# Optimization experiments

Measured on AMD Instinct MI355X. Metric: run time of the kernel, lower is better.

Reference implementation:

```python
import jax, jax.numpy as jnp
import numpy as np

N_NODES = 20000
OUT_DEG = 16
E = N_NODES * OUT_DEG          # 320000 directed edges
F = 20                          # edge_features
H3 = 3 * F


def _lin(key, fan_in, fan_out):
    kw, kb = jax.random.split(key)
    bound = 1.0 / np.sqrt(fan_in)
    W = jax.random.uniform(kw, (fan_in, fan_out), jnp.float32, -bound, bound)
    b = jax.random.uniform(kb, (fan_out,), jnp.float32, -bound, bound)
    return W, b


def setup_inputs() -> dict:
    key = jax.random.key(0)
    rng = np.random.default_rng(0)
    # graph: every node has exactly OUT_DEG out-edges, no self-loops
    src = np.repeat(np.arange(N_NODES, dtype=np.int64), OUT_DEG)
    dst = (src + 1 + rng.integers(0, N_NODES - 1, size=E)) % N_NODES
    edge_index = jnp.asarray(np.stack([src, dst]), dtype=jnp.int32)
    # edge adjacency per _build_edge_adj: edge i=(u->v) pairs with each out-edge j of v.
    # Edges are grouped by src, so out-edges of node v are [v*OUT_DEG, v*OUT_DEG+OUT_DEG).
    # No self-loops => i != j always, so exactly E*OUT_DEG pairs.
    adj_src = jnp.asarray(np.repeat(np.arange(E, dtype=np.int64), OUT_DEG).astype(np.int32))
    adj_nbr = jnp.asarray((dst[:, None] * OUT_DEG + np.arange(OUT_DEG)).reshape(-1).astype(np.int32))

    ks = jax.random.split(key, 8)
    edge_attr = jax.random.normal(ks[0], (E, F), jnp.float32)
    msg_W1, msg_b1 = _lin(ks[1], 2 * F, 32)
    msg_W2, msg_b2 = _lin(ks[2], 32, F)
    # torch GRUCell params: weight_ih/hh are [3H, H]
    bound = 1.0 / np.sqrt(F)
    g = jax.random.split(ks[3], 4)
    gru_Wih = jax.random.uniform(g[0], (H3, F), jnp.float32, -bound, bound)
    gru_Whh = jax.random.uniform(g[1], (H3, F), jnp.float32, -bound, bound)
    gru_bih = jax.random.uniform(g[2], (H3,), jnp.float32, -bound, bound)
    gru_bhh = jax.random.uniform(g[3], (H3,), jnp.float32, -bound, bound)
    ro_W1, ro_b1 = _lin(ks[4], F, 64)
    ro_W2, ro_b2 = _lin(ks[5], 64, 32)
    ro_W3, ro_b3 = _lin(ks[6], 32, 1)
    return {
        'edge_attr': edge_attr,
        'msg_W1': msg_W1, 'msg_b1': msg_b1, 'msg_W2': msg_W2, 'msg_b2': msg_b2,
        'gru_Wih': gru_Wih, 'gru_Whh': gru_Whh, 'gru_bih': gru_bih, 'gru_bhh': gru_bhh,
        'ro_W1': ro_W1, 'ro_b1': ro_b1, 'ro_W2': ro_W2, 'ro_b2': ro_b2,
        'ro_W3': ro_W3, 'ro_b3': ro_b3,
        'edge_index': edge_index, 'adj_src': adj_src, 'adj_nbr': adj_nbr,
    }


def reference(edge_attr, msg_W1, msg_b1, msg_W2, msg_b2,
              gru_Wih, gru_Whh, gru_bih, gru_bhh,
              ro_W1, ro_b1, ro_W2, ro_b2, ro_W3, ro_b3,
              edge_index, adj_src, adj_nbr):
    num_e = edge_attr.shape[0]

    def step(h, _):
        h_i = h[adj_src]                       # [P, F] gather
        h_j = h[adj_nbr]                       # [P, F] gather
        m = jnp.concatenate([h_i, h_j], axis=-1)  # [P, 2F]
        m = jax.nn.selu(m @ msg_W1 + msg_b1) @ msg_W2 + msg_b2  # [P, F]
        agg = jax.ops.segment_sum(m, adj_src, num_segments=num_e)  # scatter_add
        # torch.nn.GRUCell(agg, h)
        gi = agg @ gru_Wih.T + gru_bih
        gh = h @ gru_Whh.T + gru_bhh
        i_r, i_z, i_n = jnp.split(gi, 3, axis=-1)
        h_r, h_z, h_n = jnp.split(gh, 3, axis=-1)
        r = jax.nn.sigmoid(i_r + h_r)
        z = jax.nn.sigmoid(i_z + h_z)
        n = jnp.tanh(i_n + r * h_n)
        return (1.0 - z) * n + z * h, None

    h_t, _ = jax.lax.scan(step, edge_attr, None, length=4)
    h_base = h_t[:num_e]  # num_edges == E here
    x = jax.nn.selu(h_base @ ro_W1 + ro_b1)
    x = jax.nn.selu(x @ ro_W2 + ro_b2)
    w = jax.nn.softplus(x @ ro_W3 + ro_b3).squeeze(-1) + 0.1
    return jnp.clip(w, 0.1, 10.0)
```

## Files before the change

### kernel.cpp

```cpp
#include <hip/hip_runtime.h>
#include <hip/hip_fp16.h>

#define E_EDGES 320000
#define NF 20

typedef float v4 __attribute__((ext_vector_type(4)));
typedef float v2f __attribute__((ext_vector_type(2)));

#if defined(__has_builtin)
# if __has_builtin(__builtin_elementwise_fma)
#  define EWFMA(a,b,c) __builtin_elementwise_fma((a),(b),(c))
# endif
#endif
#ifndef EWFMA
# define EWFMA(a,b,c) ((a)*(b)+(c))
#endif
#if defined(__has_builtin)
# if __has_builtin(__builtin_elementwise_max)
#  define EWMAX(a,b) __builtin_elementwise_max((a),(b))
#  define EWMIN(a,b) __builtin_elementwise_min((a),(b))
# endif
#endif

__device__ __forceinline__ v4 bc4(float s) { return (v4){s, s, s, s}; }
__device__ __forceinline__ v4 v4z() { return (v4){0.f, 0.f, 0.f, 0.f}; }

__device__ __forceinline__ float selu_f(float x) {
    const float scale = 1.0507009873554805f;
    const float alpha = 1.6732632423543772f;
    float p = fmaxf(x, 0.f);
    float m = fminf(x, 0.f);
    float e = __expf(m);
    return fmaf(scale, p, scale * alpha * (e - 1.f));
}
__device__ __forceinline__ float sigmoid_f(float x) {
    return 1.f / (1.f + __expf(-x));
}
__device__ __forceinline__ v4 selu4(v4 x) {
    const float scale = 1.0507009873554805f;
    const float ka = 1.0507009873554805f * 1.6732632423543772f;
#ifdef EWMAX
    v4 p = EWMAX(x, v4z());
    v4 m = EWMIN(x, v4z());
#else
    v4 p = {fmaxf(x.x,0.f), fmaxf(x.y,0.f), fmaxf(x.z,0.f), fmaxf(x.w,0.f)};
    v4 m = {fminf(x.x,0.f), fminf(x.y,0.f), fminf(x.z,0.f), fminf(x.w,0.f)};
#endif
    v4 e = {__expf(m.x), __expf(m.y), __expf(m.z), __expf(m.w)};
    return EWFMA(bc4(scale), p, EWFMA(bc4(ka), e, bc4(-ka)));
}

__device__ __forceinline__ float hsum4(v4 x) {
    v2f lo = __builtin_shufflevector(x, x, 0, 1);
    v2f hi = __builtin_shufflevector(x, x, 2, 3);
    v2f h = lo + hi;
    return h.x + h.y;
}

__device__ __forceinline__ float dot20v(v4 a0, v4 a1, v4 a2, v4 a3, v4 a4,
                                        const v4* __restrict__ w) {
    v4 w0 = w[0], w1 = w[1], w2 = w[2], w3 = w[3], w4 = w[4];
    v4 x = a0 * w0;
    x = EWFMA(a1, w1, x); x = EWFMA(a2, w2, x);
    x = EWFMA(a3, w3, x); x = EWFMA(a4, w4, x);
    return hsum4(x);
}
__device__ __forceinline__ void dot20_dualv(const v4* __restrict__ w,
    v4 a0, v4 a1, v4 a2, v4 a3, v4 a4,
    v4 b0, v4 b1, v4 b2, v4 b3, v4 b4,
    float& r0, float& r1)
{
    v4 w0 = w[0], w1 = w[1], w2 = w[2], w3 = w[3], w4 = w[4];
    v4 xa = a0 * w0;
    xa = EWFMA(a1, w1, xa); xa = EWFMA(a2, w2, xa);
    xa = EWFMA(a3, w3, xa); xa = EWFMA(a4, w4, xa);
    v4 xb = b0 * w0;
    xb = EWFMA(b1, w1, xb); xb = EWFMA(b2, w2, xb);
    xb = EWFMA(b3, w3, xb); xb = EWFMA(b4, w4, xb);
    r0 = hsum4(xa);
    r1 = hsum4(xb);
}
__device__ __forceinline__ void h8_to_v4x2(uint4 r, v4& lo, v4& hi) {
    float2 fa = __half22float2(__builtin_bit_cast(__half2, r.x));
    float2 fb = __half22float2(__builtin_bit_cast(__half2, r.y));
    float2 fc = __half22float2(__builtin_bit_cast(__half2, r.z));
    float2 fd = __half22float2(__builtin_bit_cast(__half2, r.w));
    lo = (v4){fa.x, fa.y, fb.x, fb.y};
    hi = (v4){fc.x, fc.y, fd.x, fd.y};
}
__device__ __forceinline__ uint4 f8_to_h8(v4 lo, v4 hi) {
    uint4 r;
    r.x = __builtin_bit_cast(unsigned, __floats2half2_rn(lo.x, lo.y));
    r.y = __builtin_bit_cast(unsigned, __floats2half2_rn(lo.z, lo.w));
    r.z = __builtin_bit_cast(unsigned, __floats2half2_rn(hi.x, hi.y));
    r.w = __builtin_bit_cast(unsigned, __floats2half2_rn(hi.z, hi.w));
    return r;
}

#define FOR20(X) \
  X(0, v0.x) X(1, v0.y) X(2, v0.z) X(3, v0.w) \
  X(4, v1.x) X(5, v1.y) X(6, v1.z) X(7, v1.w) \
  X(8, v2.x) X(9, v2.y) X(10, v2.z) X(11, v2.w) \
  X(12, v3.x) X(13, v3.y) X(14, v3.z) X(15, v3.w) \
  X(16, v4v.x) X(17, v4v.y) X(18, v4v.z) X(19, v4v.w)

#define FOR20_2(X) \
  X(0, va0.x, vb0.x) X(1, va0.y, vb0.y) X(2, va0.z, vb0.z) X(3, va0.w, vb0.w) \
  X(4, va1.x, vb1.x) X(5, va1.y, vb1.y) X(6, va1.z, vb1.z) X(7, va1.w, vb1.w) \
  X(8, va2.x, vb2.x) X(9, va2.y, vb2.y) X(10, va2.z, vb2.z) X(11, va2.w, vb2.w) \
  X(12, va3.x, vb3.x) X(13, va3.y, vb3.y) X(14, va3.z, vb3.z) X(15, va3.w, vb3.w) \
  X(16, va4.x, vb4.x) X(17, va4.y, vb4.y) X(18, va4.z, vb4.z) X(19, va4.w, vb4.w)

#define FOR8S2(X) \
  X(0, sa0.x, sb0.x) X(1, sa0.y, sb0.y) X(2, sa0.z, sb0.z) X(3, sa0.w, sb0.w) \
  X(4, sa1.x, sb1.x) X(5, sa1.y, sb1.y) X(6, sa1.z, sb1.z) X(7, sa1.w, sb1.w)

__global__ void __launch_bounds__(256) kernel_B0(
    const float* __restrict__ h, const float* __restrict__ W1,
    const float* __restrict__ b1, __half* __restrict__ B)
{
    __shared__ __align__(16) float sw[640];
    __shared__ __align__(16) float sbias[32];
    for (int i = threadIdx.x; i < 640; i += 256) sw[i] = W1[640 + i];
    if (threadIdx.x < 32) sbias[threadIdx.x] = b1[threadIdx.x];
    __syncthreads();
    int e = blockIdx.x * 256 + threadIdx.x;
    const v4* hp = reinterpret_cast<const v4*>(h + (size_t)e * NF);
    v4 v0 = hp[0], v1 = hp[1], v2 = hp[2], v3 = hp[3], v4v = hp[4];
    const v4* bi = reinterpret_cast<const v4*>(sbias);
    v4 c0 = bi[0], c1 = bi[1], c2 = bi[2], c3 = bi[3],
       c4 = bi[4], c5 = bi[5], c6 = bi[6], c7 = bi[7];
    #define BSTEP(f, hf) { v4 t_ = bc4(hf); const v4* w_ = (const v4*)&sw[(f)*32]; \
        c0 = EWFMA(t_, w_[0], c0); c1 = EWFMA(t_, w_[1], c1); \
        c2 = EWFMA(t_, w_[2], c2); c3 = EWFMA(t_, w_[3], c3); \
        c4 = EWFMA(t_, w_[4], c4); c5 = EWFMA(t_, w_[5], c5); \
        c6 = EWFMA(t_, w_[6], c6); c7 = EWFMA(t_, w_[7], c7); }
    FOR20(BSTEP)
    #undef BSTEP
    uint4* Bp = reinterpret_cast<uint4*>(B + (size_t)e * 32);
    Bp[0] = f8_to_h8(c0, c1); Bp[1] = f8_to_h8(c2, c3);
    Bp[2] = f8_to_h8(c4, c5); Bp[3] = f8_to_h8(c6, c7);
}

__global__ void __launch_bounds__(256) kernel_step(
    const float* __restrict__ h_in, float* __restrict__ h_out,
    const __half* __restrict__ Br, const int* __restrict__ dst,
    const float* __restrict__ W1, const float* __restrict__ W2, const float* __restrict__ b2,
    const float* __restrict__ Wih, const float* __restrict__ Whh,
    const float* __restrict__ bih, const float* __restrict__ bhh)
{
    __shared__ __align__(16) float sW1[640];
    __shared__ __align__(16) float sW2[640];
    __shared__ __align__(16) float sb2v[20];
    __shared__ __align__(16) float sWih[1200];
    __shared__ __align__(16) float sWhh[1200];
    __shared__ float sbih[60];
    __shared__ float sbhh[60];
    for (int i = threadIdx.x; i < 640; i += 256) { sW1[i] = W1[i]; sW2[i] = W2[i]; }
    for (int i = threadIdx.x; i < 1200; i += 256) { sWih[i] = Wih[i]; sWhh[i] = Whh[i]; }
    if (threadIdx.x < 20) sb2v[threadIdx.x] = b2[threadIdx.x];
    else if (threadIdx.x >= 64 && threadIdx.x < 124) sbih[threadIdx.x - 64] = bih[threadIdx.x - 64];
    else if (threadIdx.x >= 128 && threadIdx.x < 188) sbhh[threadIdx.x - 128] = bhh[threadIdx.x - 128];
    __syncthreads();

    int t = blockIdx.x * 256 + threadIdx.x;
    int p = t >> 2;
    int q = t & 3;
    int ob = q * 8;
    int e0 = p * 2, e1 = p * 2 + 1;

    int2 dd = *reinterpret_cast<const int2*>(dst + e0);
    int d0 = dd.x, d1 = dd.y;

    const v4* hp0 = reinterpret_cast<const v4*>(h_in + (size_t)e0 * NF);
    const v4* hp1 = reinterpret_cast<const v4*>(h_in + (size_t)e1 * NF);
    v4 va0 = hp0[0], va1 = hp0[1], va2 = hp0[2], va3 = hp0[3], va4 = hp0[4];
    v4 vb0 = hp1[0], vb1 = hp1[1], vb2 = hp1[2], vb3 = hp1[3], vb4 = hp1[4];

    v4 aa0 = v4z(), aa1 = v4z(), ab0 = v4z(), ab1 = v4z();
    #define ASTEP2(f, h0, h1) { const v4* w_ = (const v4*)&sW1[(f)*32 + ob]; \
        v4 w0_ = w_[0], w1_ = w_[1]; \
        v4 t0_ = bc4(h0), t1_ = bc4(h1); \
        aa0 = EWFMA(t0_, w0_, aa0); aa1 = EWFMA(t0_, w1_, aa1); \
        ab0 = EWFMA(t1_, w0_, ab0); ab1 = EWFMA(t1_, w1_, ab1); }
    FOR20_2(ASTEP2)
    #undef ASTEP2

    const uint4* Bp0 = reinterpret_cast<const uint4*>(Br) + (size_t)d0 * 64 + q;
    const uint4* Bp1 = reinterpret_cast<const uint4*>(Br) + (size_t)d1 * 64 + q;
    v4 sa0 = v4z(), sa1 = v4z(), sb0 = v4z(), sb1 = v4z();
    #pragma unroll 4
    for (int k = 0; k < 16; k++) {
        uint4 rA = Bp0[k * 4];
        uint4 rB = Bp1[k * 4];
        v4 loA, hiA, loB, hiB;
        h8_to_v4x2(rA, loA, hiA);
        h8_to_v4x2(rB, loB, hiB);
        sa0 = sa0 + selu4(aa0 + loA);
        sa1 = sa1 + selu4(aa1 + hiA);
        sb0 = sb0 + selu4(ab0 + loB);
        sb1 = sb1 + selu4(ab1 + hiB);
    }

    v4 ga0 = v4z(), ga1 = v4z(), ga2 = v4z(), ga3 = v4z(), ga4 = v4z();
    v4 gb0 = v4z(), gb1 = v4z(), gb2 = v4z(), gb3 = v4z(), gb4 = v4z();
    #define AGGS2(j, c0_, c1_) { const v4* w_ = (const v4*)&sW2[(ob + (j)) * 20]; \
        v4 w0_ = w_[0], w1_ = w_[1], w2_ = w_[2], w3_ = w_[3], w4_ = w_[4]; \
        v4 u_ = bc4(c0_), vv_ = bc4(c1_); \
        ga0 = EWFMA(u_, w0_, ga0); ga1 = EWFMA(u_, w1_, ga1); ga2 = EWFMA(u_, w2_, ga2); \
        ga3 = EWFMA(u_, w3_, ga3); ga4 = EWFMA(u_, w4_, ga4); \
        gb0 = EWFMA(vv_, w0_, gb0); gb1 = EWFMA(vv_, w1_, gb1); gb2 = EWFMA(vv_, w2_, gb2); \
        gb3 = EWFMA(vv_, w3_, gb3); gb4 = EWFMA(vv_, w4_, gb4); }
    FOR8S2(AGGS2)
    #undef AGGS2

    #define BF1(r_, m_) { v4 t_ = { __shfl_xor(r_.x, m_), __shfl_xor(r_.y, m_), \
                                    __shfl_xor(r_.z, m_), __shfl_xor(r_.w, m_) }; \
                          r_ = r_ + t_; }
    #define BFLY(m_) BF1(ga0, m_) BF1(ga1, m_) BF1(ga2, m_) BF1(ga3, m_) BF1(ga4, m_) \
                     BF1(gb0, m_) BF1(gb1, m_) BF1(gb2, m_) BF1(gb3, m_) BF1(gb4, m_)
    BFLY(1)
    BFLY(2)
    #undef BFLY
    #undef BF1

    {
        const v4* b2p = reinterpret_cast<const v4*>(sb2v);
        v4 sixteen = bc4(16.f);
        v4 c0 = b2p[0], c1 = b2p[1], c2 = b2p[2], c3 = b2p[3], c4 = b2p[4];
        ga0 = EWFMA(sixteen, c0, ga0); ga1 = EWFMA(sixteen, c1, ga1); ga2 = EWFMA(sixteen, c2, ga2);
        ga3 = EWFMA(sixteen, c3, ga3); ga4 = EWFMA(sixteen, c4, ga4);
        gb0 = EWFMA(sixteen, c0, gb0); gb1 = EWFMA(sixteen, c1, gb1); gb2 = EWFMA(sixteen, c2, gb2);
        gb3 = EWFMA(sixteen, c3, gb3); gb4 = EWFMA(sixteen, c4, gb4);
    }

    for (int i = 0; i < 5; i++) {
        int c = q * 5 + i;
        float ir0, ir1, iz0, iz1, in0, in1, hr0, hr1, hz0, hz1, hn0, hn1;
        dot20_dualv((const v4*)&sWih[c * 20],        ga0, ga1, ga2, ga3, ga4,
                    gb0, gb1, gb2, gb3, gb4, ir0, ir1);
        dot20_dualv((const v4*)&sWih[(20 + c) * 20], ga0, ga1, ga2, ga3, ga4,
                    gb0, gb1, gb2, gb3, gb4, iz0, iz1);
        dot20_dualv((const v4*)&sWih[(40 + c) * 20], ga0, ga1, ga2, ga3, ga4,
                    gb0, gb1, gb2, gb3, gb4, in0, in1);
        dot20_dualv((const v4*)&sWhh[c * 20],        va0, va1, va2, va3, va4,
                    vb0, vb1, vb2, vb3, vb4, hr0, hr1);
        dot20_dualv((const v4*)&sWhh[(20 + c) * 20], va0, va1, va2, va3, va4,
                    vb0, vb1, vb2, vb3, vb4, hz0, hz1);
        dot20_dualv((const v4*)&sWhh[(40 + c) * 20], va0, va1, va2, va3, va4,
                    vb0, vb1, vb2, vb3, vb4, hn0, hn1);
        float bi_r = sbih[c], bi_z = sbih[20 + c], bi_n = sbih[40 + c];
        float bh_r = sbhh[c], bh_z = sbhh[20 + c], bh_n = sbhh[40 + c];
        {
            float r = sigmoid_f(bi_r + ir0 + bh_r + hr0);
            float z = sigmoid_f(bi_z + iz0 + bh_z + hz0);
            float xn = bi_n + in0 + r * (bh_n + hn0);
            xn = fminf(fmaxf(xn, -20.f), 20.f);
            float tt = __expf(2.f * xn);
            float n = (tt - 1.f) / (tt + 1.f);
            float hc = h_in[(size_t)e0 * NF + c];
            h_out[(size_t)e0 * NF + c] = (1.f - z) * n + z * hc;
        }
        {
            float r = sigmoid_f(bi_r + ir1 + bh_r + hr1);
            float z = sigmoid_f(bi_z + iz1 + bh_z + hz1);
            float xn = bi_n + in1 + r * (bh_n + hn1);
            xn = fminf(fmaxf(xn, -20.f), 20.f);
            float tt = __expf(2.f * xn);
            float n = (tt - 1.f) / (tt + 1.f);
            float hc = h_in[(size_t)e1 * NF + c];
            h_out[(size_t)e1 * NF + c] = (1.f - z) * n + z * hc;
        }
    }
}

__global__ void __launch_bounds__(256) kernel_readout(
    const float* __restrict__ h,
    const float* __restrict__ W1, const float* __restrict__ b1,
    const float* __restrict__ W2, const float* __restrict__ b2,
    const float* __restrict__ W3, const float* __restrict__ b3,
    float* __restrict__ out)
{
    __shared__ __align__(16) float sW1t[1280];
    __shared__ float sb1[64];
    __shared__ __align__(16) float sW2[2048];
    __shared__ __align__(16) float sb2v[32];
    __shared__ __align__(16) float sW3[32];
    __shared__ float sb3;
    for (int i = threadIdx.x; i < 1280; i += 256) {
        int f = i >> 6, o = i & 63;
        sW1t[o * 20 + f] = W1[i];
    }
    for (int i = threadIdx.x; i < 2048; i += 256) sW2[i] = W2[i];
    if (threadIdx.x < 64) sb1[threadIdx.x] = b1[threadIdx.x];
    else if (threadIdx.x >= 64 && threadIdx.x < 96) sb2v[threadIdx.x - 64] = b2[threadIdx.x - 64];
    else if (threadIdx.x >= 96 && threadIdx.x < 128) sW3[threadIdx.x - 96] = W3[threadIdx.x - 96];
    if (threadIdx.x == 128) sb3 = b3[0];
    __syncthreads();

    int e = blockIdx.x * 256 + threadIdx.x;
    const v4* hp = reinterpret_cast<const v4*>(h + (size_t)e * NF);
    v4 v0 = hp[0], v1 = hp[1], v2 = hp[2], v3 = hp[3], v4v = hp[4];

    const v4* b2p = reinterpret_cast<const v4*>(sb2v);
    v4 x20 = b2p[0], x21 = b2p[1], x22 = b2p[2], x23 = b2p[3],
       x24 = b2p[4], x25 = b2p[5], x26 = b2p[6], x27 = b2p[7];
    for (int o = 0; o < 64; o++) {
        float x1 = sb1[o] + dot20v(v0, v1, v2, v3, v4v, (const v4*)&sW1t[o * 20]);
        x1 = selu_f(x1);
        v4 xb = bc4(x1);
        const v4* w = (const v4*)&sW2[o * 32];
        x20 = EWFMA(xb, w[0], x20); x21 = EWFMA(xb, w[1], x21);
        x22 = EWFMA(xb, w[2], x22); x23 = EWFMA(xb, w[3], x23);
        x24 = EWFMA(xb, w[4], x24); x25 = EWFMA(xb, w[5], x25);
        x26 = EWFMA(xb, w[6], x26); x27 = EWFMA(xb, w[7], x27);
    }
    const v4* w3p = reinterpret_cast<const v4*>(sW3);
    v4 accv = selu4(x20) * w3p[0];
    accv = EWFMA(selu4(x21), w3p[1], accv);
    accv = EWFMA(selu4(x22), w3p[2], accv);
    accv = EWFMA(selu4(x23), w3p[3], accv);
    accv = EWFMA(selu4(x24), w3p[4], accv);
    accv = EWFMA(selu4(x25), w3p[5], accv);
    accv = EWFMA(selu4(x26), w3p[6], accv);
    accv = EWFMA(selu4(x27), w3p[7], accv);
    float acc = sb3 + hsum4(accv);
    float sp = fmaxf(acc, 0.f) + log1pf(__expf(-fabsf(acc)));
    float w = sp + 0.1f;
    w = fminf(fmaxf(w, 0.1f), 10.f);
    out[e] = w;
}

extern "C" void kernel_launch(void* const* d_in, const int* in_sizes, int n_in,
                              void* d_out, int out_size, void* d_ws, size_t ws_size,
                              hipStream_t stream) {
    const float* edge_attr = (const float*)d_in[0];
    const float* msg_W1   = (const float*)d_in[1];
    const float* msg_b1   = (const float*)d_in[2];
    const float* msg_W2   = (const float*)d_in[3];
    const float* msg_b2   = (const float*)d_in[4];
    const float* gru_Wih  = (const float*)d_in[5];
    const float* gru_Whh  = (const float*)d_in[6];
    const float* gru_bih  = (const float*)d_in[7];
    const float* gru_bhh  = (const float*)d_in[8];
    const float* ro_W1    = (const float*)d_in[9];
    const float* ro_b1    = (const float*)d_in[10];
    const float* ro_W2    = (const float*)d_in[11];
    const float* ro_b2    = (const float*)d_in[12];
    const float* ro_W3    = (const float*)d_in[13];
    const float* ro_b3    = (const float*)d_in[14];
    const int* edge_index = (const int*)d_in[15];
    const int* dst = edge_index + E_EDGES;

    float*  h_ws = (float*)d_ws;
    __half* Bt   = (__half*)(h_ws + (size_t)E_EDGES * NF);

    dim3 block(256);
    dim3 gridB(E_EDGES / 256);
    dim3 gridS(E_EDGES * 2 / 256);

    const float* hin = edge_attr;
    for (int s = 0; s < 4; s++) {
        kernel_B0<<<gridB, block, 0, stream>>>(hin, msg_W1, msg_b1, Bt);
        kernel_step<<<gridS, block, 0, stream>>>(hin, h_ws, Bt, dst,
            msg_W1, msg_W2, msg_b2, gru_Wih, gru_Whh, gru_bih, gru_bhh);
        hin = h_ws;
    }
    kernel_readout<<<gridB, block, 0, stream>>>(h_ws, ro_W1, ro_b1, ro_W2, ro_b2,
                                                ro_W3, ro_b3, (float*)d_out);
}
```

Measured before the change: 557.1 us.

## Fuse next-step B precompute into step kernel epilogue with double-buffered B

Each step kernel now computes the per-edge W1 projection for the next iteration's neighbour term in an epilogue, after a block barrier, from the h values it just wrote. The result is written to an alternating half-precision B buffer. This removes three standalone kernel_B0 launches and their extra full read of h. In exchange it adds shared memory for the second half of W1 and b1, another barrier, and a second B buffer in the workspace.

```diff
diff --git a/kernel.cpp b/kernel.cpp
--- a/kernel.cpp
+++ b/kernel.cpp
@@ -142,21 +142,30 @@
     Bp[2] = f8_to_h8(c4, c5); Bp[3] = f8_to_h8(c6, c7);
 }
 
+template<int WRITE_B>
 __global__ void __launch_bounds__(256) kernel_step(
     const float* __restrict__ h_in, float* __restrict__ h_out,
-    const __half* __restrict__ Br, const int* __restrict__ dst,
-    const float* __restrict__ W1, const float* __restrict__ W2, const float* __restrict__ b2,
+    const __half* __restrict__ Br, __half* __restrict__ Bw,
+    const int* __restrict__ dst,
+    const float* __restrict__ W1, const float* __restrict__ b1,
+    const float* __restrict__ W2, const float* __restrict__ b2,
     const float* __restrict__ Wih, const float* __restrict__ Whh,
     const float* __restrict__ bih, const float* __restrict__ bhh)
 {
     __shared__ __align__(16) float sW1[640];
+    __shared__ __align__(16) float sW1b[640];
     __shared__ __align__(16) float sW2[640];
     __shared__ __align__(16) float sb2v[20];
+    __shared__ __align__(16) float sb1v[32];
     __shared__ __align__(16) float sWih[1200];
     __shared__ __align__(16) float sWhh[1200];
     __shared__ float sbih[60];
     __shared__ float sbhh[60];
     for (int i = threadIdx.x; i < 640; i += 256) { sW1[i] = W1[i]; sW2[i] = W2[i]; }
+    if (WRITE_B) {
+        for (int i = threadIdx.x; i < 640; i += 256) sW1b[i] = W1[640 + i];
+        if (threadIdx.x >= 192 && threadIdx.x < 224) sb1v[threadIdx.x - 192] = b1[threadIdx.x - 192];
+    }
     for (int i = threadIdx.x; i < 1200; i += 256) { sWih[i] = Wih[i]; sWhh[i] = Whh[i]; }
     if (threadIdx.x < 20) sb2v[threadIdx.x] = b2[threadIdx.x];
     else if (threadIdx.x >= 64 && threadIdx.x < 124) sbih[threadIdx.x - 64] = bih[threadIdx.x - 64];
@@ -272,6 +281,28 @@
             h_out[(size_t)e1 * NF + c] = (1.f - z) * n + z * hc;
         }
     }
+
+    if (WRITE_B) {
+        __syncthreads();
+        const v4* b1p = (const v4*)&sb1v[ob];
+        v4 bbA0 = b1p[0], bbA1 = b1p[1];
+        v4 bbB0 = bbA0, bbB1 = bbA1;
+        const float* ho0 = h_out + (size_t)e0 * NF;
+        const float* ho1 = h_out + (size_t)e1 * NF;
+        #pragma unroll
+        for (int f = 0; f < 20; f++) {
+            float hf0 = ho0[f];
+            float hf1 = ho1[f];
+            const v4* w_ = (const v4*)&sW1b[f * 32 + ob];
+            v4 w0 = w_[0], w1 = w_[1];
+            v4 t0 = bc4(hf0), t1 = bc4(hf1);
+            bbA0 = EWFMA(t0, w0, bbA0); bbA1 = EWFMA(t0, w1, bbA1);
+            bbB0 = EWFMA(t1, w0, bbB0); bbB1 = EWFMA(t1, w1, bbB1);
+        }
+        uint4* bw = reinterpret_cast<uint4*>(Bw);
+        bw[(size_t)e0 * 4 + q] = f8_to_h8(bbA0, bbA1);
+        bw[(size_t)e1 * 4 + q] = f8_to_h8(bbB0, bbB1);
+    }
 }
 
 __global__ void __launch_bounds__(256) kernel_readout(
@@ -353,19 +384,23 @@
     const int* dst = edge_index + E_EDGES;
 
     float*  h_ws = (float*)d_ws;
-    __half* Bt   = (__half*)(h_ws + (size_t)E_EDGES * NF);
+    __half* B0b  = (__half*)(h_ws + (size_t)E_EDGES * NF);
+    __half* B1b  = B0b + (size_t)E_EDGES * 32;
 
     dim3 block(256);
     dim3 gridB(E_EDGES / 256);
     dim3 gridS(E_EDGES * 2 / 256);
 
-    const float* hin = edge_attr;
-    for (int s = 0; s < 4; s++) {
-        kernel_B0<<<gridB, block, 0, stream>>>(hin, msg_W1, msg_b1, Bt);
-        kernel_step<<<gridS, block, 0, stream>>>(hin, h_ws, Bt, dst,
-            msg_W1, msg_W2, msg_b2, gru_Wih, gru_Whh, gru_bih, gru_bhh);
-        hin = h_ws;
-    }
+    kernel_B0<<<gridB, block, 0, stream>>>(edge_attr, msg_W1, msg_b1, B0b);
+    kernel_step<1><<<gridS, block, 0, stream>>>(edge_attr, h_ws, B0b, B1b, dst,
+        msg_W1, msg_b1, msg_W2, msg_b2, gru_Wih, gru_Whh, gru_bih, gru_bhh);
+    kernel_step<1><<<gridS, block, 0, stream>>>(h_ws, h_ws, B1b, B0b, dst,
+        msg_W1, msg_b1, msg_W2, msg_b2, gru_Wih, gru_Whh, gru_bih, gru_bhh);
+    kernel_step<1><<<gridS, block, 0, stream>>>(h_ws, h_ws, B0b, B1b, dst,
+        msg_W1, msg_b1, msg_W2, msg_b2, gru_Wih, gru_Whh, gru_bih, gru_bhh);
+    kernel_step<0><<<gridS, block, 0, stream>>>(h_ws, h_ws, B1b, B0b, dst,
+        msg_W1, msg_b1, msg_W2, msg_b2, gru_Wih, gru_Whh, gru_bih, gru_bhh);
+
     kernel_readout<<<gridB, block, 0, stream>>>(h_ws, ro_W1, ro_b1, ro_W2, ro_b2,
                                                 ro_W3, ro_b3, (float*)d_out);
 }
```

New measurement: 587.3 us. 1.05x slower.

## Process edges in destination-sorted order to improve gather locality

Applied to the files above, without the earlier changes.

Adds a counting-sort prologue (zero, histogram, scan, scatter) that builds a permutation of edges grouped by destination node. The step kernel then processes edges in that order, so neighbouring threads read the same B rows for a node's out-edges and get better cache reuse. The cost is four extra small kernel launches, including a single-block scan, plus scattered reads of h_in and writes of h_out in permuted order. The order from the atomic scatter is nondeterministic, but each edge's result still lands at its own index.

```diff
diff --git a/kernel.cpp b/kernel.cpp
--- a/kernel.cpp
+++ b/kernel.cpp
@@ -2,6 +2,7 @@
 #include <hip/hip_fp16.h>
 
 #define E_EDGES 320000
+#define N_NODES 20000
 #define NF 20
 
 typedef float v4 __attribute__((ext_vector_type(4)));
@@ -22,23 +23,25 @@
 # endif
 #endif
 
+#define SELU_S 1.0507009873554805f
+#define SELU_KA (1.0507009873554805f * 1.6732632423543772f)
+
 __device__ __forceinline__ v4 bc4(float s) { return (v4){s, s, s, s}; }
 __device__ __forceinline__ v4 v4z() { return (v4){0.f, 0.f, 0.f, 0.f}; }
 
 __device__ __forceinline__ float selu_f(float x) {
-    const float scale = 1.0507009873554805f;
-    const float alpha = 1.6732632423543772f;
     float p = fmaxf(x, 0.f);
     float m = fminf(x, 0.f);
     float e = __expf(m);
-    return fmaf(scale, p, scale * alpha * (e - 1.f));
+    return fmaf(SELU_S, p, SELU_KA * (e - 1.f));
 }
 __device__ __forceinline__ float sigmoid_f(float x) {
     return 1.f / (1.f + __expf(-x));
 }
+__device__ __forceinline__ v4 exp4(v4 m) {
+    return (v4){__expf(m.x), __expf(m.y), __expf(m.z), __expf(m.w)};
+}
 __device__ __forceinline__ v4 selu4(v4 x) {
-    const float scale = 1.0507009873554805f;
-    const float ka = 1.0507009873554805f * 1.6732632423543772f;
 #ifdef EWMAX
     v4 p = EWMAX(x, v4z());
     v4 m = EWMIN(x, v4z());
@@ -46,8 +49,7 @@
     v4 p = {fmaxf(x.x,0.f), fmaxf(x.y,0.f), fmaxf(x.z,0.f), fmaxf(x.w,0.f)};
     v4 m = {fminf(x.x,0.f), fminf(x.y,0.f), fminf(x.z,0.f), fminf(x.w,0.f)};
 #endif
-    v4 e = {__expf(m.x), __expf(m.y), __expf(m.z), __expf(m.w)};
-    return EWFMA(bc4(scale), p, EWFMA(bc4(ka), e, bc4(-ka)));
+    return EWFMA(bc4(SELU_S), p, EWFMA(bc4(SELU_KA), exp4(m), bc4(-SELU_KA)));
 }
 
 __device__ __forceinline__ float hsum4(v4 x) {
@@ -114,6 +116,48 @@
 #define FOR8S2(X) \
   X(0, sa0.x, sb0.x) X(1, sa0.y, sb0.y) X(2, sa0.z, sb0.z) X(3, sa0.w, sb0.w) \
   X(4, sa1.x, sb1.x) X(5, sa1.y, sb1.y) X(6, sa1.z, sb1.z) X(7, sa1.w, sb1.w)
+
+__global__ void __launch_bounds__(256) kernel_zero(int* __restrict__ hist) {
+    int i = blockIdx.x * 256 + threadIdx.x;
+    if (i < N_NODES) hist[i] = 0;
+}
+__global__ void __launch_bounds__(256) kernel_hist(
+    const int* __restrict__ dst, int* __restrict__ hist) {
+    int e = blockIdx.x * 256 + threadIdx.x;
+    atomicAdd(&hist[dst[e]], 1);
+}
+__global__ void __launch_bounds__(1024) kernel_scan(
+    const int* __restrict__ hist, int* __restrict__ ofs) {
+    __shared__ int buf[1024];
+    __shared__ int carry;
+    if (threadIdx.x == 0) carry = 0;
+    __syncthreads();
+    for (int base = 0; base < N_NODES; base += 1024) {
+        int i = base + threadIdx.x;
+        int v = (i < N_NODES) ? hist[i] : 0;
+        buf[threadIdx.x] = v;
+        __syncthreads();
+        for (int off = 1; off < 1024; off <<= 1) {
+            int t = (threadIdx.x >= off) ? buf[threadIdx.x - off] : 0;
+            __syncthreads();
+            buf[threadIdx.x] += t;
+            __syncthreads();
+        }
+        if (i < N_NODES) ofs[i] = buf[threadIdx.x] - v + carry;
+        __syncthreads();
+        if (threadIdx.x == 1023) carry += buf[1023];
+        __syncthreads();
+    }
+}
+__global__ void __launch_bounds__(256) kernel_scatter(
+    const int* __restrict__ dst, int* __restrict__ ofs,
+    int* __restrict__ perm, int* __restrict__ sdst) {
+    int e = blockIdx.x * 256 + threadIdx.x;
+    int d = dst[e];
+    int pos = atomicAdd(&ofs[d], 1);
+    perm[pos] = e;
+    sdst[pos] = d;
+}
 
 __global__ void __launch_bounds__(256) kernel_B0(
     const float* __restrict__ h, const float* __restrict__ W1,
@@ -144,7 +188,8 @@
 
 __global__ void __launch_bounds__(256) kernel_step(
     const float* __restrict__ h_in, float* __restrict__ h_out,
-    const __half* __restrict__ Br, const int* __restrict__ dst,
+    const __half* __restrict__ Br,
+    const int* __restrict__ perm, const int* __restrict__ sdst,
     const float* __restrict__ W1, const float* __restrict__ W2, const float* __restrict__ b2,
     const float* __restrict__ Wih, const float* __restrict__ Whh,
     const float* __restrict__ bih, const float* __restrict__ bhh)
@@ -167,9 +212,10 @@
     int p = t >> 2;
     int q = t & 3;
     int ob = q * 8;
-    int e0 = p * 2, e1 = p * 2 + 1;
-
-    int2 dd = *reinterpret_cast<const int2*>(dst + e0);
+
+    int2 pe = *reinterpret_cast<const int2*>(perm + p * 2);
+    int2 dd = *reinterpret_cast<const int2*>(sdst + p * 2);
+    int e0 = pe.x, e1 = pe.y;
     int d0 = dd.x, d1 = dd.y;
 
     const v4* hp0 = reinterpret_cast<const v4*>(h_in + (size_t)e0 * NF);
@@ -354,15 +400,25 @@
 
     float*  h_ws = (float*)d_ws;
     __half* Bt   = (__half*)(h_ws + (size_t)E_EDGES * NF);
+    int*    perm = (int*)(Bt + (size_t)E_EDGES * 32);
+    int*    sdst = perm + E_EDGES;
+    int*    hist = sdst + E_EDGES;
+    int*    ofs  = hist + N_NODES;
 
     dim3 block(256);
     dim3 gridB(E_EDGES / 256);
     dim3 gridS(E_EDGES * 2 / 256);
+    dim3 gridZ((N_NODES + 255) / 256);
+
+    kernel_zero<<<gridZ, block, 0, stream>>>(hist);
+    kernel_hist<<<gridB, block, 0, stream>>>(dst, hist);
+    kernel_scan<<<1, 1024, 0, stream>>>(hist, ofs);
+    kernel_scatter<<<gridB, block, 0, stream>>>(dst, ofs, perm, sdst);
 
     const float* hin = edge_attr;
     for (int s = 0; s < 4; s++) {
         kernel_B0<<<gridB, block, 0, stream>>>(hin, msg_W1, msg_b1, Bt);
-        kernel_step<<<gridS, block, 0, stream>>>(hin, h_ws, Bt, dst,
+        kernel_step<<<gridS, block, 0, stream>>>(hin, h_ws, Bt, perm, sdst,
             msg_W1, msg_W2, msg_b2, gru_Wih, gru_Whh, gru_bih, gru_bhh);
         hin = h_ws;
     }
```

After: 674.9 us. 1.21x slower.
